# Kernel optimization log

Hardware: AMD Instinct MI355X
Metric: run time of the kernel (lower is better)

The kernel has to match this reference:

```python
import jax, jax.numpy as jnp
import numpy as np

EPS = 1e-08


def setup_inputs() -> dict:
    key = jax.random.key(0)
    X = jax.random.normal(key, (16384, 768), dtype=jnp.float32)
    return {"X": X}


def reference(X) -> jnp.ndarray:
    # L2-normalize rows (torch F.normalize with eps: divide by max(norm, eps))
    norms = jnp.linalg.norm(X, axis=-1, keepdims=True)
    Xn = X / jnp.maximum(norms, EPS)

    n = Xn.shape[0]
    # pairwise inner products [n, n]; mask self-similarity on diagonal with -1
    dots = Xn @ Xn.T
    dots = jnp.where(jnp.eye(n, dtype=bool), jnp.float32(-1.0), dots)
    I = jnp.argmax(dots, axis=1)  # nearest neighbor index per row

    # torch PairwiseDistance(2, eps): ||x - y + eps||_2
    diff = Xn - Xn[I] + EPS
    distances = jnp.linalg.norm(diff, axis=-1)

    # loss_type == 'standard'
    loss = -jnp.mean(jnp.log(distances + EPS))
    return loss
```

## Files before the change

kernel.cpp:

```cpp
#include <hip/hip_runtime.h>
#include <hip/hip_bf16.h>
#include <stdint.h>
#include <math.h>

#define NR 16384
#define DIM 768
#define KEPS 1e-8f

#define BM 128
#define NB (NR / BM)
#define KT (DIM / 64)
#define NQ (DIM / 16)
#define NTILES (NB * (NB + 1) / 2)

typedef __attribute__((ext_vector_type(4))) float f32x4;
typedef __attribute__((ext_vector_type(2))) long long2_t;

__device__ inline uint32_t fkey(float f) {
    union { float f; uint32_t u; } v; v.f = f;
    return (v.u & 0x80000000u) ? ~v.u : (v.u | 0x80000000u);
}

__device__ inline unsigned long long pack_vc(float v, int c) {
    return ((unsigned long long)fkey(v) << 32) | (unsigned)c;
}

__device__ inline uint8_t f2fp8(float f) {
    union { float f; uint32_t u; } v; v.f = f;
    const uint8_t s = (uint8_t)((v.u >> 24) & 0x80u);
    float a = fabsf(f);
    if (a >= 448.0f) return s | 0x7E;
    if (a < 0.015625f) {
        int q = (int)rintf(a * 512.0f);
        if (q >= 8) return s | 0x08;
        return s | (uint8_t)q;
    }
    int ex; float m = frexpf(a, &ex);
    int E = ex + 6;
    int frac = (int)rintf(m * 16.0f - 8.0f);
    if (frac >= 8) { frac = 0; ++E; if (E > 15) return s | 0x7E; }
    return s | (uint8_t)(E << 3) | (uint8_t)frac;
}

__global__ __launch_bounds__(256) void k_norm(const float* __restrict__ X,
                                              uint8_t* __restrict__ XnT,
                                              float* __restrict__ norms) {
    __shared__ uint8_t buf[4][768];
    const int wid = threadIdx.x >> 6, lane = threadIdx.x & 63;
    const int row = blockIdx.x * 4 + wid;
    const float4* xr = (const float4*)(X + (size_t)row * DIM) + lane * 3;
    float4 a = xr[0], b = xr[1], c = xr[2];
    float s = a.x*a.x + a.y*a.y + a.z*a.z + a.w*a.w
            + b.x*b.x + b.y*b.y + b.z*b.z + b.w*b.w
            + c.x*c.x + c.y*c.y + c.z*c.z + c.w*c.w;
#pragma unroll
    for (int m = 32; m >= 1; m >>= 1) s += __shfl_xor(s, m);
    const float n = sqrtf(s);
    if (lane == 0) norms[row] = n;
    const float rn = 1.0f / fmaxf(n, KEPS);
    float v[12] = {a.x,a.y,a.z,a.w,b.x,b.y,b.z,b.w,c.x,c.y,c.z,c.w};
    uint8_t q[12];
#pragma unroll
    for (int i = 0; i < 12; ++i) q[i] = f2fp8(v[i] * rn);
    uint32_t* lb = (uint32_t*)&buf[wid][lane * 12];
    lb[0] = (uint32_t)q[0] | ((uint32_t)q[1] << 8) | ((uint32_t)q[2]  << 16) | ((uint32_t)q[3]  << 24);
    lb[1] = (uint32_t)q[4] | ((uint32_t)q[5] << 8) | ((uint32_t)q[6]  << 16) | ((uint32_t)q[7]  << 24);
    lb[2] = (uint32_t)q[8] | ((uint32_t)q[9] << 8) | ((uint32_t)q[10] << 16) | ((uint32_t)q[11] << 24);
    __syncthreads();
    if (lane < NQ) {
        const int blk = lane >> 2;
        const int h   = lane & 3;
        const uint2 lo = *(const uint2*)&buf[wid][blk * 64 + h * 8];
        const uint2 hi = *(const uint2*)&buf[wid][blk * 64 + 32 + h * 8];
        const size_t off = ((size_t)(row >> 7) * NQ * 128 + (size_t)lane * 128
                            + (row & 127)) * 16;
        *(uint4*)(XnT + off) = make_uint4(lo.x, lo.y, hi.x, hi.y);
    }
}

__global__ __launch_bounds__(256) void k_init(unsigned long long* __restrict__ nn64) {
    nn64[blockIdx.x * 256 + threadIdx.x] = pack_vc(-2.0f, 0);
}

__global__ __launch_bounds__(256, 3) void k_maxdot(const uint8_t* __restrict__ XnT,
                                                   unsigned long long* __restrict__ nn64) {
    const int tid  = threadIdx.x;
    const int lane = tid & 63, wid = tid >> 6;
    const int wr = wid >> 1, wc = wid & 1;
    const int l15 = lane & 15, lhi = lane >> 4;

    int t = (int)blockIdx.x;
    t = (t & 7) * (NTILES / 8) + (t >> 3);
    float disc = 66049.0f - 8.0f * (float)t;
    int rb = (int)((257.0f - sqrtf(disc)) * 0.5f);
    if (rb > NB - 1) rb = NB - 1;
    if (rb < 0) rb = 0;
    while (rb > 0 && rb * (257 - rb) / 2 > t) --rb;
    while ((rb + 1) * (257 - (rb + 1)) / 2 <= t) ++rb;
    const int cb = rb + (t - rb * (257 - rb) / 2);
    const int rowbase = rb * BM;
    const int colbase = cb * BM;
    const bool diag = (rb == cb);

    const uint8_t* pA = XnT + (size_t)rb * NQ * 128 * 16;
    const uint8_t* pB = XnT + (size_t)cb * NQ * 128 * 16;

    f32x4 acc[4][4];
    const f32x4 z = {0.f, 0.f, 0.f, 0.f};
#pragma unroll
    for (int i = 0; i < 4; ++i)
#pragma unroll
        for (int j = 0; j < 4; ++j) acc[i][j] = z;

    const int arow = wr * 64 + l15;
    const int brow = wc * 64 + l15;
#pragma unroll 2
    for (int kt = 0; kt < KT; ++kt) {
        const size_t qoff = (size_t)(kt * 4 + lhi) * 128 * 16;
        long2_t af[4], bg[4];
#pragma unroll
        for (int mf = 0; mf < 4; ++mf)
            af[mf] = *(const long2_t*)(pA + qoff + (size_t)(arow + mf * 16) * 16);
#pragma unroll
        for (int nf = 0; nf < 4; ++nf)
            bg[nf] = *(const long2_t*)(pB + qoff + (size_t)(brow + nf * 16) * 16);
#pragma unroll
        for (int mf = 0; mf < 4; ++mf)
#pragma unroll
            for (int nf = 0; nf < 4; ++nf)
                acc[mf][nf] = __builtin_amdgcn_mfma_f32_16x16x32_fp8_fp8(
                    af[mf].x, bg[nf].x, acc[mf][nf], 0, 0, 0);
#pragma unroll
        for (int mf = 0; mf < 4; ++mf)
#pragma unroll
            for (int nf = 0; nf < 4; ++nf)
                acc[mf][nf] = __builtin_amdgcn_mfma_f32_16x16x32_fp8_fp8(
                    af[mf].y, bg[nf].y, acc[mf][nf], 0, 0, 0);
    }

    if (diag) {
#pragma unroll
        for (int mf = 0; mf < 4; ++mf)
#pragma unroll
            for (int nf = 0; nf < 4; ++nf)
#pragma unroll
                for (int rr = 0; rr < 4; ++rr) {
                    const int rl = wr * 64 + mf * 16 + lhi * 4 + rr;
                    const int cl = wc * 64 + nf * 16 + l15;
                    if (rl == cl) acc[mf][nf][rr] = -1.0f;
                }
    }

#pragma unroll
    for (int mf = 0; mf < 4; ++mf)
#pragma unroll
        for (int rr = 0; rr < 4; ++rr) {
            float v = acc[mf][0][rr];
            int   c = colbase + wc * 64 + l15;
#pragma unroll
            for (int nf = 1; nf < 4; ++nf) {
                const float w2 = acc[mf][nf][rr];
                const int   c2 = colbase + wc * 64 + nf * 16 + l15;
                if (w2 > v) { v = w2; c = c2; }
            }
#pragma unroll
            for (int m = 1; m <= 8; m <<= 1) {
                const float ov = __shfl_xor(v, m);
                const int   oc = __shfl_xor(c, m);
                if (ov > v) { v = ov; c = oc; }
            }
            if (l15 == 0) {
                const int r = rowbase + wr * 64 + mf * 16 + lhi * 4 + rr;
                atomicMax(&nn64[r], pack_vc(v, c));
            }
        }

#pragma unroll
    for (int nf = 0; nf < 4; ++nf) {
        float v = acc[0][nf][0];
        int   c = rowbase + wr * 64 + lhi * 4;
#pragma unroll
        for (int mf = 0; mf < 4; ++mf)
#pragma unroll
            for (int rr = 0; rr < 4; ++rr) {
                if (mf == 0 && rr == 0) continue;
                const float w2 = acc[mf][nf][rr];
                const int   c2 = rowbase + wr * 64 + mf * 16 + lhi * 4 + rr;
                if (w2 > v) { v = w2; c = c2; }
            }
#pragma unroll
        for (int m = 16; m <= 32; m <<= 1) {
            const float ov = __shfl_xor(v, m);
            const int   oc = __shfl_xor(c, m);
            if (ov > v) { v = ov; c = oc; }
        }
        if ((lane >> 4) == 0) {
            const int cc = colbase + wc * 64 + nf * 16 + l15;
            atomicMax(&nn64[cc], pack_vc(v, c));
        }
    }
}

__global__ __launch_bounds__(256) void k_refine(const float* __restrict__ X,
                                                const float* __restrict__ norms,
                                                const unsigned long long* __restrict__ nn64,
                                                float* __restrict__ logd) {
    const int wid = threadIdx.x >> 6, lane = threadIdx.x & 63;
    const int r = blockIdx.x * 4 + wid;
    const int j = (int)(nn64[r] & 0xFFFFu);
    const float rnr = 1.0f / fmaxf(norms[r], KEPS);
    const float rnj = 1.0f / fmaxf(norms[j], KEPS);
    const float4* xr = (const float4*)(X + (size_t)r * DIM) + lane * 3;
    const float4* xj = (const float4*)(X + (size_t)j * DIM) + lane * 3;
    float s = 0.0f;
#pragma unroll
    for (int i = 0; i < 3; ++i) {
        const float4 a = xr[i], b = xj[i];
        float d;
        d = a.x * rnr - b.x * rnj + KEPS; s = fmaf(d, d, s);
        d = a.y * rnr - b.y * rnj + KEPS; s = fmaf(d, d, s);
        d = a.z * rnr - b.z * rnj + KEPS; s = fmaf(d, d, s);
        d = a.w * rnr - b.w * rnj + KEPS; s = fmaf(d, d, s);
    }
#pragma unroll
    for (int m = 32; m >= 1; m >>= 1) s += __shfl_xor(s, m);
    if (lane == 0) logd[r] = logf(sqrtf(s) + KEPS);
}

__global__ __launch_bounds__(256) void k_loss(const float* __restrict__ logd,
                                              float* __restrict__ out) {
    float local = 0.0f;
    for (int r = threadIdx.x; r < NR; r += 256) local += logd[r];
#pragma unroll
    for (int m = 32; m >= 1; m >>= 1) local += __shfl_xor(local, m);
    __shared__ float red[4];
    const int lane = threadIdx.x & 63, wid = threadIdx.x >> 6;
    if (lane == 0) red[wid] = local;
    __syncthreads();
    if (threadIdx.x == 0)
        out[0] = -(red[0] + red[1] + red[2] + red[3]) / (float)NR;
}

extern "C" void kernel_launch(void* const* d_in, const int* in_sizes, int n_in,
                              void* d_out, int out_size, void* d_ws, size_t ws_size,
                              hipStream_t stream) {
    const float* X = (const float*)d_in[0];
    float* out = (float*)d_out;
    uint8_t* XnT = (uint8_t*)d_ws;
    char* p = (char*)d_ws + (size_t)NR * DIM;
    float* norms = (float*)p;                 p += (size_t)NR * 4;
    unsigned long long* nn64 = (unsigned long long*)p; p += (size_t)NR * 8;
    float* logd = (float*)p;

    k_norm<<<NR / 4, 256, 0, stream>>>(X, XnT, norms);
    k_init<<<NR / 256, 256, 0, stream>>>(nn64);
    k_maxdot<<<NTILES, 256, 0, stream>>>(XnT, nn64);
    k_refine<<<NR / 4, 256, 0, stream>>>(X, norms, nn64, logd);
    k_loss<<<1, 256, 0, stream>>>(logd, out);
}
```

Baseline: 307.9 us.

## Double-buffer fragment loads in maxdot and batch 64 rows per norm block

Result: slower. 431.6 us (+40.2%).

```diff
diff --git a/kernel.cpp b/kernel.cpp
--- a/kernel.cpp
+++ b/kernel.cpp
@@ -9,7 +9,6 @@
 
 #define BM 128
 #define NB (NR / BM)
-#define KT (DIM / 64)
 #define NQ (DIM / 16)
 #define NTILES (NB * (NB + 1) / 2)
 
@@ -45,41 +44,70 @@
 __global__ __launch_bounds__(256) void k_norm(const float* __restrict__ X,
                                               uint8_t* __restrict__ XnT,
                                               float* __restrict__ norms) {
-    __shared__ uint8_t buf[4][768];
+    __shared__ uint8_t buf[64][776];
     const int wid = threadIdx.x >> 6, lane = threadIdx.x & 63;
-    const int row = blockIdx.x * 4 + wid;
-    const float4* xr = (const float4*)(X + (size_t)row * DIM) + lane * 3;
-    float4 a = xr[0], b = xr[1], c = xr[2];
-    float s = a.x*a.x + a.y*a.y + a.z*a.z + a.w*a.w
-            + b.x*b.x + b.y*b.y + b.z*b.z + b.w*b.w
-            + c.x*c.x + c.y*c.y + c.z*c.z + c.w*c.w;
-#pragma unroll
-    for (int m = 32; m >= 1; m >>= 1) s += __shfl_xor(s, m);
-    const float n = sqrtf(s);
-    if (lane == 0) norms[row] = n;
-    const float rn = 1.0f / fmaxf(n, KEPS);
-    float v[12] = {a.x,a.y,a.z,a.w,b.x,b.y,b.z,b.w,c.x,c.y,c.z,c.w};
-    uint8_t q[12];
-#pragma unroll
-    for (int i = 0; i < 12; ++i) q[i] = f2fp8(v[i] * rn);
-    uint32_t* lb = (uint32_t*)&buf[wid][lane * 12];
-    lb[0] = (uint32_t)q[0] | ((uint32_t)q[1] << 8) | ((uint32_t)q[2]  << 16) | ((uint32_t)q[3]  << 24);
-    lb[1] = (uint32_t)q[4] | ((uint32_t)q[5] << 8) | ((uint32_t)q[6]  << 16) | ((uint32_t)q[7]  << 24);
-    lb[2] = (uint32_t)q[8] | ((uint32_t)q[9] << 8) | ((uint32_t)q[10] << 16) | ((uint32_t)q[11] << 24);
+#pragma unroll
+    for (int i = 0; i < 16; ++i) {
+        const int rloc = wid * 16 + i;
+        const int grow = blockIdx.x * 64 + rloc;
+        const float4* xr = (const float4*)(X + (size_t)grow * DIM) + lane * 3;
+        float4 a = xr[0], b = xr[1], c = xr[2];
+        float s = a.x*a.x + a.y*a.y + a.z*a.z + a.w*a.w
+                + b.x*b.x + b.y*b.y + b.z*b.z + b.w*b.w
+                + c.x*c.x + c.y*c.y + c.z*c.z + c.w*c.w;
+#pragma unroll
+        for (int m = 32; m >= 1; m >>= 1) s += __shfl_xor(s, m);
+        const float n = sqrtf(s);
+        if (lane == 0) norms[grow] = n;
+        const float rn = 1.0f / fmaxf(n, KEPS);
+        float v[12] = {a.x,a.y,a.z,a.w,b.x,b.y,b.z,b.w,c.x,c.y,c.z,c.w};
+        uint8_t q[12];
+#pragma unroll
+        for (int k = 0; k < 12; ++k) q[k] = f2fp8(v[k] * rn);
+        uint32_t* lb = (uint32_t*)&buf[rloc][lane * 12];
+        lb[0] = (uint32_t)q[0] | ((uint32_t)q[1] << 8) | ((uint32_t)q[2]  << 16) | ((uint32_t)q[3]  << 24);
+        lb[1] = (uint32_t)q[4] | ((uint32_t)q[5] << 8) | ((uint32_t)q[6]  << 16) | ((uint32_t)q[7]  << 24);
+        lb[2] = (uint32_t)q[8] | ((uint32_t)q[9] << 8) | ((uint32_t)q[10] << 16) | ((uint32_t)q[11] << 24);
+    }
     __syncthreads();
-    if (lane < NQ) {
-        const int blk = lane >> 2;
-        const int h   = lane & 3;
-        const uint2 lo = *(const uint2*)&buf[wid][blk * 64 + h * 8];
-        const uint2 hi = *(const uint2*)&buf[wid][blk * 64 + 32 + h * 8];
-        const size_t off = ((size_t)(row >> 7) * NQ * 128 + (size_t)lane * 128
-                            + (row & 127)) * 16;
+    const int r  = threadIdx.x & 63;
+    const int qg = threadIdx.x >> 6;
+    const int p   = blockIdx.x >> 1;
+    const int rip = (blockIdx.x & 1) * 64 + r;
+#pragma unroll
+    for (int i = 0; i < 12; ++i) {
+        const int q = i * 4 + qg;
+        const int blk = q >> 2, h = q & 3;
+        const uint2 lo = *(const uint2*)&buf[r][blk * 64 + h * 8];
+        const uint2 hi = *(const uint2*)&buf[r][blk * 64 + 32 + h * 8];
+        const size_t off = ((size_t)p * NQ * 128 + (size_t)q * 128 + rip) * 16;
         *(uint4*)(XnT + off) = make_uint4(lo.x, lo.y, hi.x, hi.y);
     }
 }
 
 __global__ __launch_bounds__(256) void k_init(unsigned long long* __restrict__ nn64) {
     nn64[blockIdx.x * 256 + threadIdx.x] = pack_vc(-2.0f, 0);
+}
+
+__device__ __forceinline__ void mstep(f32x4 (&acc)[4][4],
+                                      long2_t a0, long2_t a1, long2_t a2, long2_t a3,
+                                      long2_t b0, long2_t b1, long2_t b2, long2_t b3) {
+    const long ax[4] = {a0.x, a1.x, a2.x, a3.x};
+    const long ay[4] = {a0.y, a1.y, a2.y, a3.y};
+    const long bx[4] = {b0.x, b1.x, b2.x, b3.x};
+    const long by[4] = {b0.y, b1.y, b2.y, b3.y};
+#pragma unroll
+    for (int mf = 0; mf < 4; ++mf)
+#pragma unroll
+        for (int nf = 0; nf < 4; ++nf)
+            acc[mf][nf] = __builtin_amdgcn_mfma_f32_16x16x32_fp8_fp8(
+                ax[mf], bx[nf], acc[mf][nf], 0, 0, 0);
+#pragma unroll
+    for (int mf = 0; mf < 4; ++mf)
+#pragma unroll
+        for (int nf = 0; nf < 4; ++nf)
+            acc[mf][nf] = __builtin_amdgcn_mfma_f32_16x16x32_fp8_fp8(
+                ay[mf], by[nf], acc[mf][nf], 0, 0, 0);
 }
 
 __global__ __launch_bounds__(256, 3) void k_maxdot(const uint8_t* __restrict__ XnT,
@@ -114,29 +142,31 @@
 
     const int arow = wr * 64 + l15;
     const int brow = wc * 64 + l15;
-#pragma unroll 2
-    for (int kt = 0; kt < KT; ++kt) {
-        const size_t qoff = (size_t)(kt * 4 + lhi) * 128 * 16;
-        long2_t af[4], bg[4];
-#pragma unroll
-        for (int mf = 0; mf < 4; ++mf)
-            af[mf] = *(const long2_t*)(pA + qoff + (size_t)(arow + mf * 16) * 16);
-#pragma unroll
-        for (int nf = 0; nf < 4; ++nf)
-            bg[nf] = *(const long2_t*)(pB + qoff + (size_t)(brow + nf * 16) * 16);
-#pragma unroll
-        for (int mf = 0; mf < 4; ++mf)
-#pragma unroll
-            for (int nf = 0; nf < 4; ++nf)
-                acc[mf][nf] = __builtin_amdgcn_mfma_f32_16x16x32_fp8_fp8(
-                    af[mf].x, bg[nf].x, acc[mf][nf], 0, 0, 0);
-#pragma unroll
-        for (int mf = 0; mf < 4; ++mf)
-#pragma unroll
-            for (int nf = 0; nf < 4; ++nf)
-                acc[mf][nf] = __builtin_amdgcn_mfma_f32_16x16x32_fp8_fp8(
-                    af[mf].y, bg[nf].y, acc[mf][nf], 0, 0, 0);
-    }
+
+    long2_t aA0, aA1, aA2, aA3, bA0, bA1, bA2, bA3;
+    long2_t aB0, aB1, aB2, aB3, bB0, bB1, bB2, bB3;
+
+#define LOADN(P, KT) do {                                                   \
+        const size_t qo_ = (size_t)((KT) * 4 + lhi) * 2048;                 \
+        a##P##0 = *(const long2_t*)(pA + qo_ + (size_t)(arow     ) * 16);   \
+        a##P##1 = *(const long2_t*)(pA + qo_ + (size_t)(arow + 16) * 16);   \
+        a##P##2 = *(const long2_t*)(pA + qo_ + (size_t)(arow + 32) * 16);   \
+        a##P##3 = *(const long2_t*)(pA + qo_ + (size_t)(arow + 48) * 16);   \
+        b##P##0 = *(const long2_t*)(pB + qo_ + (size_t)(brow     ) * 16);   \
+        b##P##1 = *(const long2_t*)(pB + qo_ + (size_t)(brow + 16) * 16);   \
+        b##P##2 = *(const long2_t*)(pB + qo_ + (size_t)(brow + 32) * 16);   \
+        b##P##3 = *(const long2_t*)(pB + qo_ + (size_t)(brow + 48) * 16);   \
+    } while (0)
+
+    LOADN(A, 0);
+#pragma unroll
+    for (int kt2 = 0; kt2 < 6; ++kt2) {
+        LOADN(B, kt2 * 2 + 1);
+        mstep(acc, aA0, aA1, aA2, aA3, bA0, bA1, bA2, bA3);
+        if (kt2 < 5) LOADN(A, kt2 * 2 + 2);
+        mstep(acc, aB0, aB1, aB2, aB3, bB0, bB1, bB2, bB3);
+    }
+#undef LOADN
 
     if (diag) {
 #pragma unroll
@@ -252,7 +282,7 @@
     unsigned long long* nn64 = (unsigned long long*)p; p += (size_t)NR * 8;
     float* logd = (float*)p;
 
-    k_norm<<<NR / 4, 256, 0, stream>>>(X, XnT, norms);
+    k_norm<<<NR / 64, 256, 0, stream>>>(X, XnT, norms);
     k_init<<<NR / 256, 256, 0, stream>>>(nn64);
     k_maxdot<<<NTILES, 256, 0, stream>>>(XnT, nn64);
     k_refine<<<NR / 4, 256, 0, stream>>>(X, norms, nn64, logd);
```
